# Optimization experiments

Measured on AMD Instinct MI355X. Metric: run time of the kernel, lower is better.

The kernel has to match this reference:

```python
import jax, jax.numpy as jnp
import numpy as np
import math

D_MODEL = 1024
NUM_HEADS = 16
D_K = D_MODEL // NUM_HEADS
SEQ_LEN = 2048
THETA = 10000.0


def _rope_tables(seq_len, d_k, theta):
    # inv_freq over even dims, angles repeated-interleaved to full d_k
    inv_freq = theta ** (-jnp.arange(0, d_k, 2, dtype=jnp.float32) / d_k)  # [d_k/2]
    pos = jnp.arange(seq_len, dtype=jnp.float32)                          # [s]
    angles = pos[:, None] * inv_freq[None, :]                             # [s, d_k/2]
    angles = jnp.repeat(angles, 2, axis=-1)                               # [s, d_k]
    return jnp.cos(angles), jnp.sin(angles)


def _rotate_half(x):
    # interleaved pairs: (x0,x1,x2,x3,...) -> (-x1,x0,-x3,x2,...)
    x_even = x[..., ::2]
    x_odd = x[..., 1::2]
    return jnp.stack([-x_odd, x_even], axis=-1).reshape(x.shape)


def _apply_rope(x, cos, sin):
    # x: [b, h, s, d_k]; cos/sin: [s, d_k]
    return x * cos + _rotate_half(x) * sin


def setup_inputs() -> dict:
    key = jax.random.key(0)
    ks = jax.random.split(key, 5)
    scale = 1.0 / math.sqrt(D_MODEL)
    X = jax.random.normal(ks[0], (2, SEQ_LEN, D_MODEL), dtype=jnp.float32)
    Wq = jax.random.normal(ks[1], (D_MODEL, D_MODEL), dtype=jnp.float32) * scale
    Wk = jax.random.normal(ks[2], (D_MODEL, D_MODEL), dtype=jnp.float32) * scale
    Wv = jax.random.normal(ks[3], (D_MODEL, D_MODEL), dtype=jnp.float32) * scale
    Wo = jax.random.normal(ks[4], (D_MODEL, D_MODEL), dtype=jnp.float32) * scale
    return {"X": X, "Wq": Wq, "Wk": Wk, "Wv": Wv, "Wo": Wo}


def reference(X, Wq, Wk, Wv, Wo):
    b, s, _ = X.shape
    h, dk = NUM_HEADS, D_K

    def proj(W):
        return (X @ W.T).reshape(b, s, h, dk).transpose(0, 2, 1, 3)  # [b,h,s,dk]

    q, k, v = proj(Wq), proj(Wk), proj(Wv)

    cos, sin = _rope_tables(s, dk, THETA)
    q = _apply_rope(q, cos, sin)
    k = _apply_rope(k, cos, sin)

    scores = jnp.einsum('bhid,bhjd->bhij', q, k) / math.sqrt(dk)
    causal = jnp.tril(jnp.ones((s, s), dtype=bool))
    scores = jnp.where(causal[None, None], scores, -jnp.inf)
    probs = jax.nn.softmax(scores, axis=-1)
    attended = jnp.einsum('bhij,bhjd->bhid', probs, v)               # [b,h,s,dk]

    out = attended.transpose(0, 2, 1, 3).reshape(b, s, h * dk)
    return out @ Wo.T
```

## Files before the change

kernel.cpp:

```cpp
#include <hip/hip_runtime.h>
#include <stdint.h>

#define D_MODEL 1024
#define NUM_HEADS 16
#define DK 64
#define SEQ 2048
#define BATCH 2
#define MROWS (BATCH * SEQ)
#define LOG2E 1.4426950408889634f
#define FIXM 14.0f

typedef short bf16x8 __attribute__((ext_vector_type(8)));
typedef float f32x4 __attribute__((ext_vector_type(4)));
typedef float f32x16 __attribute__((ext_vector_type(16)));

__device__ __forceinline__ unsigned short f2bf(float f) {
    unsigned int u = __float_as_uint(f);
    u = (u + 0x7fffu + ((u >> 16) & 1u)) >> 16;
    return (unsigned short)u;
}
__device__ __forceinline__ unsigned short f2bf_trunc(float f) {
    return (unsigned short)(__float_as_uint(f) >> 16);
}
__device__ __forceinline__ float bf2f(unsigned short h) {
    return __uint_as_float(((unsigned int)h) << 16);
}
__device__ __forceinline__ void async16(const void* g, void* l) {
    __builtin_amdgcn_global_load_lds(
        (const __attribute__((address_space(1))) void*)g,
        (__attribute__((address_space(3))) void*)l, 16, 0, 0);
}
#define SWZ64(row, b) ((((row) * 8) + ((b) ^ ((row) & 7))) * 8)

__global__ void cast_all(const float4* __restrict__ X, const float4* __restrict__ Wq,
                         const float4* __restrict__ Wk, const float4* __restrict__ Wv,
                         const float4* __restrict__ Wo, ushort4* __restrict__ Xb,
                         ushort4* __restrict__ Wqkvb, ushort4* __restrict__ Wob) {
    int i = blockIdx.x * blockDim.x + threadIdx.x;
    const float4* src;
    ushort4* dst;
    int off;
    if (i < 1048576) { src = X; dst = Xb; off = i; }
    else if (i < 1310720) { src = Wq; dst = Wqkvb; off = i - 1048576; }
    else if (i < 1572864) { src = Wk; dst = Wqkvb + 262144; off = i - 1310720; }
    else if (i < 1835008) { src = Wv; dst = Wqkvb + 524288; off = i - 1572864; }
    else { src = Wo; dst = Wob; off = i - 1835008; }
    float4 v = src[off];
    ushort4 o;
    o.x = f2bf(v.x); o.y = f2bf(v.y); o.z = f2bf(v.z); o.w = f2bf(v.w);
    dst[off] = o;
}

template <int TN, int OUT_BF16>
__global__ __launch_bounds__(256) void gemm_tile(
    const unsigned short* __restrict__ A, const unsigned short* __restrict__ B,
    void* __restrict__ Cout, int M, int N, int K) {
    __shared__ unsigned short As[128 * 64];
    __shared__ unsigned short Bs[TN * 64];
    const int m0 = blockIdx.y * 128, n0 = blockIdx.x * TN;
    const int t = threadIdx.x;
    const int lane = t & 63, wave = t >> 6;
    const int mA = lane & 15, quad = lane >> 4;
    constexpr int MI = (TN == 128) ? 4 : 2;
    constexpr int NI = 4;
    const int wr = (TN == 128) ? (wave >> 1) * 64 : wave * 32;
    const int wc = (TN == 128) ? (wave & 1) * 64 : 0;

    f32x4 acc[MI][NI] = {};
    for (int k0 = 0; k0 < K; k0 += 64) {
#pragma unroll
        for (int i = 0; i < 4; ++i) {
            int ch = i * 256 + t;
            int r = ch >> 3, b = (ch & 7) ^ (r & 7);
            async16(A + (size_t)(m0 + r) * K + k0 + b * 8, (char*)As + ch * 16);
        }
#pragma unroll
        for (int i = 0; i < TN / 32; ++i) {
            int ch = i * 256 + t;
            int r = ch >> 3, b = (ch & 7) ^ (r & 7);
            async16(B + (size_t)(n0 + r) * K + k0 + b * 8, (char*)Bs + ch * 16);
        }
        __syncthreads();
#pragma unroll
        for (int kk = 0; kk < 2; ++kk) {
            bf16x8 af[MI], bfr[NI];
#pragma unroll
            for (int mi = 0; mi < MI; ++mi) {
                int rr = wr + mi * 16 + mA;
                af[mi] = *(const bf16x8*)&As[SWZ64(rr, kk * 4 + quad)];
            }
#pragma unroll
            for (int ni = 0; ni < NI; ++ni) {
                int rr = wc + ni * 16 + mA;
                bfr[ni] = *(const bf16x8*)&Bs[SWZ64(rr, kk * 4 + quad)];
            }
#pragma unroll
            for (int mi = 0; mi < MI; ++mi)
#pragma unroll
                for (int ni = 0; ni < NI; ++ni)
                    acc[mi][ni] = __builtin_amdgcn_mfma_f32_16x16x32_bf16(
                        af[mi], bfr[ni], acc[mi][ni], 0, 0, 0);
        }
        __syncthreads();
    }
#pragma unroll
    for (int mi = 0; mi < MI; ++mi)
#pragma unroll
        for (int ni = 0; ni < NI; ++ni)
#pragma unroll
            for (int r = 0; r < 4; ++r) {
                int gm = m0 + wr + mi * 16 + quad * 4 + r;
                int gn = n0 + wc + ni * 16 + mA;
                if (OUT_BF16)
                    ((unsigned short*)Cout)[(size_t)gm * N + gn] = f2bf(acc[mi][ni][r]);
                else
                    ((float*)Cout)[(size_t)gm * N + gn] = acc[mi][ni][r];
            }
}

__global__ __launch_bounds__(256) void rope_vt(const unsigned short* __restrict__ QKV,
                                               unsigned short* __restrict__ Qr,
                                               unsigned short* __restrict__ Kr,
                                               unsigned short* __restrict__ Vt) {
    __shared__ unsigned short T[64][80];
    const int bx = blockIdx.x;
    const int t = threadIdx.x;
    if (bx < 4096) {
        int tid = bx * 256 + t;
        int bs = tid >> 8;
        int p4 = tid & 255;
        int b = bs >> 11, spos = bs & 2047;
        int h = p4 >> 4, dd = (p4 & 15) * 4;
        float sn0, cs0, sn1, cs1;
        {
            float if0 = __expf(-(float)dd * (9.210340371976184f / 64.0f));
            float if1 = __expf(-(float)(dd + 2) * (9.210340371976184f / 64.0f));
            __sincosf((float)spos * if0, &sn0, &cs0);
            __sincosf((float)spos * if1, &sn1, &cs1);
        }
        size_t src = (size_t)bs * 3072 + h * 64 + dd;
        ushort4 qw = *(const ushort4*)&QKV[src];
        ushort4 kw = *(const ushort4*)&QKV[src + 1024];
        ushort4 qo_, ko_;
        float e = bf2f(qw.x), o = bf2f(qw.y);
        qo_.x = f2bf(e * cs0 - o * sn0); qo_.y = f2bf(o * cs0 + e * sn0);
        e = bf2f(qw.z); o = bf2f(qw.w);
        qo_.z = f2bf(e * cs1 - o * sn1); qo_.w = f2bf(o * cs1 + e * sn1);
        e = bf2f(kw.x); o = bf2f(kw.y);
        ko_.x = f2bf(e * cs0 - o * sn0); ko_.y = f2bf(o * cs0 + e * sn0);
        e = bf2f(kw.z); o = bf2f(kw.w);
        ko_.z = f2bf(e * cs1 - o * sn1); ko_.w = f2bf(o * cs1 + e * sn1);
        size_t qb = (((size_t)(b * NUM_HEADS + h) * SEQ + spos) * DK + dd);
        *(ushort4*)&Qr[qb] = qo_;
        *(ushort4*)&Kr[qb] = ko_;
    } else {
        int idx = bx - 4096;
        const int s0 = (idx & 31) * 64, bh = idx >> 5;
        const int b = bh >> 4, h = bh & 15;
#pragma unroll
        for (int i = 0; i < 2; ++i) {
            int ch = i * 256 + t;
            int row = ch >> 3, bc = ch & 7;
            *(int4*)&T[row][bc * 8] =
                *(const int4*)&QKV[(size_t)(b * SEQ + s0 + row) * 3072 + 2048 + h * 64 + bc * 8];
        }
        __syncthreads();
#pragma unroll
        for (int i = 0; i < 2; ++i) {
            int ch = i * 256 + t;
            int d = ch >> 3, sb = ch & 7;
            unsigned short tmp[8];
#pragma unroll
            for (int j = 0; j < 8; ++j) tmp[j] = T[sb * 8 + j][d];
            *(int4*)&Vt[(size_t)bh * DK * SEQ + (size_t)d * SEQ + s0 + sb * 8] = *(int4*)tmp;
        }
    }
}

__global__ __launch_bounds__(256, 2) void flash_attn7(
    const unsigned short* __restrict__ Qr, const unsigned short* __restrict__ Kr,
    const unsigned short* __restrict__ Vt, unsigned short* __restrict__ Att) {
    __shared__ unsigned short Ks[2][64 * 64];
    __shared__ unsigned short Vs[2][64 * 64];
    __shared__ unsigned short Ps[4][32 * 64];
    const int bh = blockIdx.x;
    const int qt = 15 - (int)blockIdx.y;
    const int t = threadIdx.x;
    const int lane = t & 63, wave = t >> 6;
    const int l31 = lane & 31, lh = lane >> 5;
    const int qb = qt * 128 + wave * 32;
    const size_t qkbase = (size_t)bh * SEQ * DK;
    const unsigned short* Kg = Kr + qkbase;
    const unsigned short* Vg = Vt + (size_t)bh * DK * SEQ;
    const int jtmax = 2 * qt + 1;

    bf16x8 aq[4];
#pragma unroll
    for (int kk = 0; kk < 4; ++kk) {
        bf16x8 raw = *(const bf16x8*)&Qr[qkbase + (size_t)(qb + l31) * DK + kk * 16 + lh * 8];
        bf16x8 s;
#pragma unroll
        for (int j = 0; j < 8; ++j)
            s[j] = (short)f2bf(bf2f((unsigned short)raw[j]) * (0.125f * LOG2E));
        aq[kk] = s;
    }

    f32x16 accT[2];
#pragma unroll
    for (int ti = 0; ti < 2; ++ti)
#pragma unroll
        for (int r = 0; r < 16; ++r) accT[ti][r] = 0.f;
    float lsum[16];
#pragma unroll
    for (int r = 0; r < 16; ++r) lsum[r] = 0.f;

#pragma unroll
    for (int i = 0; i < 2; ++i) {
        int ch = i * 256 + t;
        int row = ch >> 3, sb = (ch & 7) ^ (row & 7);
        async16(Kg + (size_t)row * DK + sb * 8, (char*)Ks[0] + ch * 16);
        async16(Vg + (size_t)row * SEQ + sb * 8, (char*)Vs[0] + ch * 16);
    }

    unsigned short* Pw = Ps[wave];
    for (int jt = 0; jt <= jtmax; ++jt) {
        __syncthreads();
        const int cur = jt & 1;
        if (jt < jtmax) {
            const int j1 = (jt + 1) * 64;
#pragma unroll
            for (int i = 0; i < 2; ++i) {
                int ch = i * 256 + t;
                int row = ch >> 3, sb = (ch & 7) ^ (row & 7);
                async16(Kg + (size_t)(j1 + row) * DK + sb * 8, (char*)Ks[cur ^ 1] + ch * 16);
                async16(Vg + (size_t)row * SEQ + j1 + sb * 8, (char*)Vs[cur ^ 1] + ch * 16);
            }
        }
        const int j0 = jt * 64;
        if (j0 > qb + 31) continue;
        const unsigned short* Kt = Ks[cur];
        const unsigned short* Vtile = Vs[cur];
        const bool straddle = (j0 + 63 > qb);

#pragma unroll
        for (int ni = 0; ni < 2; ++ni) {
            f32x16 sc;
#pragma unroll
            for (int r = 0; r < 16; ++r) sc[r] = 0.f;
            __builtin_amdgcn_s_setprio(1);
#pragma unroll
            for (int kk = 0; kk < 4; ++kk) {
                bf16x8 kf = *(const bf16x8*)&Kt[SWZ64(ni * 32 + l31, kk * 2 + lh)];
                sc = __builtin_amdgcn_mfma_f32_32x32x16_bf16(aq[kk], kf, sc, 0, 0, 0);
            }
            __builtin_amdgcn_s_setprio(0);
            const int jg = j0 + ni * 32 + l31;
            if (straddle) {
#pragma unroll
                for (int r = 0; r < 16; ++r) {
                    int ql = (r & 3) + 8 * (r >> 2) + 4 * lh;
                    if (jg > qb + ql) sc[r] = -1e30f;
                }
            }
#pragma unroll
            for (int r = 0; r < 16; ++r) {
                float p = __builtin_amdgcn_exp2f(sc[r] - FIXM);
                lsum[r] += p;
                int ql = (r & 3) + 8 * (r >> 2) + 4 * lh;
                Pw[SWZ64(ql, ni * 4 + (l31 >> 3)) + (lane & 7)] = f2bf_trunc(p);
            }
        }

        bf16x8 ap[4];
#pragma unroll
        for (int kk = 0; kk < 4; ++kk)
            ap[kk] = *(const bf16x8*)&Pw[SWZ64(l31, kk * 2 + lh)];
        __builtin_amdgcn_s_setprio(1);
#pragma unroll
        for (int ti = 0; ti < 2; ++ti)
#pragma unroll
            for (int kk = 0; kk < 4; ++kk) {
                bf16x8 vf = *(const bf16x8*)&Vtile[SWZ64(ti * 32 + l31, kk * 2 + lh)];
                accT[ti] = __builtin_amdgcn_mfma_f32_32x32x16_bf16(vf, ap[kk], accT[ti], 0, 0, 0);
            }
        __builtin_amdgcn_s_setprio(0);
    }

#pragma unroll
    for (int r = 0; r < 16; ++r)
#pragma unroll
        for (int off = 1; off < 32; off <<= 1)
            lsum[r] += __shfl_xor(lsum[r], off, 64);
    __syncthreads();
    float* LL = (float*)Ks;
    if (l31 == 0)
#pragma unroll
        for (int r = 0; r < 16; ++r)
            LL[wave * 32 + (r & 3) + 8 * (r >> 2) + 4 * lh] = lsum[r];
    __syncthreads();
    const float rl = 1.0f / LL[wave * 32 + l31];

    const int b = bh >> 4, h = bh & 15;
    const int qg = qb + l31;
#pragma unroll
    for (int ti = 0; ti < 2; ++ti)
#pragma unroll
        for (int rg = 0; rg < 4; ++rg) {
            ushort4 o;
            o.x = f2bf(accT[ti][rg * 4 + 0] * rl);
            o.y = f2bf(accT[ti][rg * 4 + 1] * rl);
            o.z = f2bf(accT[ti][rg * 4 + 2] * rl);
            o.w = f2bf(accT[ti][rg * 4 + 3] * rl);
            *(ushort4*)&Att[(size_t)(b * SEQ + qg) * D_MODEL + h * DK + ti * 32 + 8 * rg + 4 * lh] = o;
        }
}

extern "C" void kernel_launch(void* const* d_in, const int* in_sizes, int n_in,
                              void* d_out, int out_size, void* d_ws, size_t ws_size,
                              hipStream_t stream) {
    const float* X = (const float*)d_in[0];
    const float* Wq = (const float*)d_in[1];
    const float* Wk = (const float*)d_in[2];
    const float* Wv = (const float*)d_in[3];
    const float* Wo = (const float*)d_in[4];

    char* ws = (char*)d_ws;
    unsigned short* Xb     = (unsigned short*)(ws + 0);
    unsigned short* Wqkvb  = (unsigned short*)(ws + (8u << 20));
    unsigned short* Wob    = (unsigned short*)(ws + (14u << 20));
    unsigned short* QKVraw = (unsigned short*)(ws + (16u << 20));
    unsigned short* Kr     = (unsigned short*)(ws + (40u << 20));
    unsigned short* Vt     = (unsigned short*)(ws + (48u << 20));
    unsigned short* Qr     = Xb;
    unsigned short* Att    = QKVraw;

    cast_all<<<8192, 256, 0, stream>>>((const float4*)X, (const float4*)Wq,
                                       (const float4*)Wk, (const float4*)Wv,
                                       (const float4*)Wo, (ushort4*)Xb,
                                       (ushort4*)Wqkvb, (ushort4*)Wob);

    gemm_tile<128, 1><<<dim3(3072 / 128, MROWS / 128), 256, 0, stream>>>(
        Xb, Wqkvb, QKVraw, MROWS, 3072, D_MODEL);

    rope_vt<<<4096 + 1024, 256, 0, stream>>>(QKVraw, Qr, Kr, Vt);

    flash_attn7<<<dim3(BATCH * NUM_HEADS, 16), 256, 0, stream>>>(Qr, Kr, Vt, Att);

    gemm_tile<64, 0><<<dim3(D_MODEL / 64, MROWS / 128), 256, 0, stream>>>(
        Att, Wob, d_out, MROWS, D_MODEL, D_MODEL);
}
```

Before: 190.0 us.

## Pair causal query tiles per block and split KV columns across waves

The flash attention kernel now gives each block two 64-row query tiles (pr and 31-pr), so every block does the same amount of causal work. Inside a block, waves split 2x2 over query halves and KV column halves. Each wave's P tile is shared through LDS with the sibling wave, and the softmax denominators are combined across the pair. The Q scaling by 0.125*log2e moves into the RoPE kernel, which removes the per-element rescale when Q is loaded. In exchange there is an extra barrier per KV tile, the output is written twice per block, and diagonal tiles take a more complex masking path.

```diff
diff --git a/kernel.cpp b/kernel.cpp
--- a/kernel.cpp
+++ b/kernel.cpp
@@ -138,14 +138,17 @@
             __sincosf((float)spos * if0, &sn0, &cs0);
             __sincosf((float)spos * if1, &sn1, &cs1);
         }
+        const float SCQ = 0.125f * LOG2E;
+        float cs0q = cs0 * SCQ, sn0q = sn0 * SCQ;
+        float cs1q = cs1 * SCQ, sn1q = sn1 * SCQ;
         size_t src = (size_t)bs * 3072 + h * 64 + dd;
         ushort4 qw = *(const ushort4*)&QKV[src];
         ushort4 kw = *(const ushort4*)&QKV[src + 1024];
         ushort4 qo_, ko_;
         float e = bf2f(qw.x), o = bf2f(qw.y);
-        qo_.x = f2bf(e * cs0 - o * sn0); qo_.y = f2bf(o * cs0 + e * sn0);
+        qo_.x = f2bf(e * cs0q - o * sn0q); qo_.y = f2bf(o * cs0q + e * sn0q);
         e = bf2f(qw.z); o = bf2f(qw.w);
-        qo_.z = f2bf(e * cs1 - o * sn1); qo_.w = f2bf(o * cs1 + e * sn1);
+        qo_.z = f2bf(e * cs1q - o * sn1q); qo_.w = f2bf(o * cs1q + e * sn1q);
         e = bf2f(kw.x); o = bf2f(kw.y);
         ko_.x = f2bf(e * cs0 - o * sn0); ko_.y = f2bf(o * cs0 + e * sn0);
         e = bf2f(kw.z); o = bf2f(kw.w);
@@ -177,39 +180,37 @@
     }
 }
 
-__global__ __launch_bounds__(256, 2) void flash_attn7(
+__global__ __launch_bounds__(256, 2) void flash_attn8(
     const unsigned short* __restrict__ Qr, const unsigned short* __restrict__ Kr,
     const unsigned short* __restrict__ Vt, unsigned short* __restrict__ Att) {
     __shared__ unsigned short Ks[2][64 * 64];
     __shared__ unsigned short Vs[2][64 * 64];
-    __shared__ unsigned short Ps[4][32 * 64];
+    __shared__ unsigned short Ps[2][32 * 64];
     const int bh = blockIdx.x;
-    const int qt = 15 - (int)blockIdx.y;
+    const int pr = blockIdx.y;
     const int t = threadIdx.x;
     const int lane = t & 63, wave = t >> 6;
     const int l31 = lane & 31, lh = lane >> 5;
-    const int qb = qt * 128 + wave * 32;
+    const int wq = wave >> 1, wj = wave & 1;
     const size_t qkbase = (size_t)bh * SEQ * DK;
     const unsigned short* Kg = Kr + qkbase;
     const unsigned short* Vg = Vt + (size_t)bh * DK * SEQ;
-    const int jtmax = 2 * qt + 1;
+    const int qtA = pr, qtB = 31 - pr;
+    const int itA = qtA + 1, itTot = qtA + qtB + 2;
+    unsigned short* PB = Ps[wq];
+    const int b_ = bh >> 4, h_ = bh & 15;
+
+    int qt = qtA;
+    int qb = qt * 64 + wq * 32;
 
     bf16x8 aq[4];
 #pragma unroll
-    for (int kk = 0; kk < 4; ++kk) {
-        bf16x8 raw = *(const bf16x8*)&Qr[qkbase + (size_t)(qb + l31) * DK + kk * 16 + lh * 8];
-        bf16x8 s;
-#pragma unroll
-        for (int j = 0; j < 8; ++j)
-            s[j] = (short)f2bf(bf2f((unsigned short)raw[j]) * (0.125f * LOG2E));
-        aq[kk] = s;
-    }
-
-    f32x16 accT[2];
-#pragma unroll
-    for (int ti = 0; ti < 2; ++ti)
-#pragma unroll
-        for (int r = 0; r < 16; ++r) accT[ti][r] = 0.f;
+    for (int kk = 0; kk < 4; ++kk)
+        aq[kk] = *(const bf16x8*)&Qr[qkbase + (size_t)(qb + l31) * DK + kk * 16 + lh * 8];
+
+    f32x16 accT;
+#pragma unroll
+    for (int r = 0; r < 16; ++r) accT[r] = 0.f;
     float lsum[16];
 #pragma unroll
     for (int r = 0; r < 16; ++r) lsum[r] = 0.f;
@@ -222,12 +223,13 @@
         async16(Vg + (size_t)row * SEQ + sb * 8, (char*)Vs[0] + ch * 16);
     }
 
-    unsigned short* Pw = Ps[wave];
-    for (int jt = 0; jt <= jtmax; ++jt) {
+    for (int it = 0; it < itTot; ++it) {
+        const int jt = (it >= itA) ? it - itA : it;
         __syncthreads();
-        const int cur = jt & 1;
-        if (jt < jtmax) {
-            const int j1 = (jt + 1) * 64;
+        const int cur = it & 1;
+        if (it + 1 < itTot) {
+            const int njt = (it + 1 >= itA) ? it + 1 - itA : it + 1;
+            const int j1 = njt * 64;
 #pragma unroll
             for (int i = 0; i < 2; ++i) {
                 int ch = i * 256 + t;
@@ -236,30 +238,26 @@
                 async16(Vg + (size_t)row * SEQ + j1 + sb * 8, (char*)Vs[cur ^ 1] + ch * 16);
             }
         }
-        const int j0 = jt * 64;
-        if (j0 > qb + 31) continue;
         const unsigned short* Kt = Ks[cur];
         const unsigned short* Vtile = Vs[cur];
-        const bool straddle = (j0 + 63 > qb);
-
-#pragma unroll
-        for (int ni = 0; ni < 2; ++ni) {
+        const int diag = (jt == qt);
+
+        if (!(diag && wq == 0 && wj == 1)) {
             f32x16 sc;
 #pragma unroll
             for (int r = 0; r < 16; ++r) sc[r] = 0.f;
             __builtin_amdgcn_s_setprio(1);
 #pragma unroll
             for (int kk = 0; kk < 4; ++kk) {
-                bf16x8 kf = *(const bf16x8*)&Kt[SWZ64(ni * 32 + l31, kk * 2 + lh)];
+                bf16x8 kf = *(const bf16x8*)&Kt[SWZ64(wj * 32 + l31, kk * 2 + lh)];
                 sc = __builtin_amdgcn_mfma_f32_32x32x16_bf16(aq[kk], kf, sc, 0, 0, 0);
             }
             __builtin_amdgcn_s_setprio(0);
-            const int jg = j0 + ni * 32 + l31;
-            if (straddle) {
+            if (diag && wj == wq) {
 #pragma unroll
                 for (int r = 0; r < 16; ++r) {
                     int ql = (r & 3) + 8 * (r >> 2) + 4 * lh;
-                    if (jg > qb + ql) sc[r] = -1e30f;
+                    if (l31 > ql) sc[r] = -1e30f;
                 }
             }
 #pragma unroll
@@ -267,52 +265,58 @@
                 float p = __builtin_amdgcn_exp2f(sc[r] - FIXM);
                 lsum[r] += p;
                 int ql = (r & 3) + 8 * (r >> 2) + 4 * lh;
-                Pw[SWZ64(ql, ni * 4 + (l31 >> 3)) + (lane & 7)] = f2bf_trunc(p);
-            }
-        }
-
-        bf16x8 ap[4];
-#pragma unroll
-        for (int kk = 0; kk < 4; ++kk)
-            ap[kk] = *(const bf16x8*)&Pw[SWZ64(l31, kk * 2 + lh)];
+                PB[SWZ64(ql, wj * 4 + (l31 >> 3)) + (l31 & 7)] = f2bf_trunc(p);
+            }
+        }
+        asm volatile("s_waitcnt lgkmcnt(0)" ::: "memory");
+        __builtin_amdgcn_s_barrier();
+        asm volatile("" ::: "memory");
+        __builtin_amdgcn_sched_barrier(0);
+
+        const int kmax = (diag && wq == 0) ? 2 : 4;
         __builtin_amdgcn_s_setprio(1);
-#pragma unroll
-        for (int ti = 0; ti < 2; ++ti)
-#pragma unroll
-            for (int kk = 0; kk < 4; ++kk) {
-                bf16x8 vf = *(const bf16x8*)&Vtile[SWZ64(ti * 32 + l31, kk * 2 + lh)];
-                accT[ti] = __builtin_amdgcn_mfma_f32_32x32x16_bf16(vf, ap[kk], accT[ti], 0, 0, 0);
-            }
+        for (int kk = 0; kk < kmax; ++kk) {
+            bf16x8 ap = *(const bf16x8*)&PB[SWZ64(l31, kk * 2 + lh)];
+            bf16x8 vf = *(const bf16x8*)&Vtile[SWZ64(wj * 32 + l31, kk * 2 + lh)];
+            accT = __builtin_amdgcn_mfma_f32_32x32x16_bf16(vf, ap, accT, 0, 0, 0);
+        }
         __builtin_amdgcn_s_setprio(0);
+
+        if (it == itA - 1 || it == itTot - 1) {
+#pragma unroll
+            for (int r = 0; r < 16; ++r)
+#pragma unroll
+                for (int off = 1; off < 32; off <<= 1)
+                    lsum[r] += __shfl_xor(lsum[r], off, 64);
+            __syncthreads();
+            float* LP = (float*)Ps;
+            if (l31 == 0)
+#pragma unroll
+                for (int r = 0; r < 16; ++r)
+                    LP[(wq * 2 + wj) * 32 + (r & 3) + 8 * (r >> 2) + 4 * lh] = lsum[r];
+            __syncthreads();
+            const float rl = 1.0f / (LP[wq * 64 + l31] + LP[wq * 64 + 32 + l31]);
+            const int qg = qb + l31;
+#pragma unroll
+            for (int rg = 0; rg < 4; ++rg) {
+                ushort4 o;
+                o.x = f2bf(accT[rg * 4 + 0] * rl);
+                o.y = f2bf(accT[rg * 4 + 1] * rl);
+                o.z = f2bf(accT[rg * 4 + 2] * rl);
+                o.w = f2bf(accT[rg * 4 + 3] * rl);
+                *(ushort4*)&Att[(size_t)(b_ * SEQ + qg) * D_MODEL + h_ * DK + wj * 32 + 8 * rg + 4 * lh] = o;
+            }
+            if (it == itA - 1) {
+                qt = qtB;
+                qb = qt * 64 + wq * 32;
+#pragma unroll
+                for (int kk = 0; kk < 4; ++kk)
+                    aq[kk] = *(const bf16x8*)&Qr[qkbase + (size_t)(qb + l31) * DK + kk * 16 + lh * 8];
+#pragma unroll
+                for (int r = 0; r < 16; ++r) { accT[r] = 0.f; lsum[r] = 0.f; }
+            }
+        }
     }
-
-#pragma unroll
-    for (int r = 0; r < 16; ++r)
-#pragma unroll
-        for (int off = 1; off < 32; off <<= 1)
-            lsum[r] += __shfl_xor(lsum[r], off, 64);
-    __syncthreads();
-    float* LL = (float*)Ks;
-    if (l31 == 0)
-#pragma unroll
-        for (int r = 0; r < 16; ++r)
-            LL[wave * 32 + (r & 3) + 8 * (r >> 2) + 4 * lh] = lsum[r];
-    __syncthreads();
-    const float rl = 1.0f / LL[wave * 32 + l31];
-
-    const int b = bh >> 4, h = bh & 15;
-    const int qg = qb + l31;
-#pragma unroll
-    for (int ti = 0; ti < 2; ++ti)
-#pragma unroll
-        for (int rg = 0; rg < 4; ++rg) {
-            ushort4 o;
-            o.x = f2bf(accT[ti][rg * 4 + 0] * rl);
-            o.y = f2bf(accT[ti][rg * 4 + 1] * rl);
-            o.z = f2bf(accT[ti][rg * 4 + 2] * rl);
-            o.w = f2bf(accT[ti][rg * 4 + 3] * rl);
-            *(ushort4*)&Att[(size_t)(b * SEQ + qg) * D_MODEL + h * DK + ti * 32 + 8 * rg + 4 * lh] = o;
-        }
 }
 
 extern "C" void kernel_launch(void* const* d_in, const int* in_sizes, int n_in,
@@ -344,7 +348,7 @@
 
     rope_vt<<<4096 + 1024, 256, 0, stream>>>(QKVraw, Qr, Kr, Vt);
 
-    flash_attn7<<<dim3(BATCH * NUM_HEADS, 16), 256, 0, stream>>>(Qr, Kr, Vt, Att);
+    flash_attn8<<<dim3(BATCH * NUM_HEADS, 16), 256, 0, stream>>>(Qr, Kr, Vt, Att);
 
     gemm_tile<64, 0><<<dim3(D_MODEL / 64, MROWS / 128), 256, 0, stream>>>(
         Att, Wob, d_out, MROWS, D_MODEL, D_MODEL);
```

After: 185.9 us. 1.02x faster.
